# Kernel tuning notes

Hardware: AMD Instinct MI355X
Metric: run time of the kernel (lower is better)

## Reference

```python
import jax, jax.numpy as jnp
import numpy as np

D_IN = 3072      # == d_out (code reshapes x directly into heads)
D_OUT = 3072
N_HEADS = 16
HEAD_DIM = D_OUT // N_HEADS          # 192
D_C = D_OUT // 3                     # 1024, compressed latent dim
LN_EPS = 1e-5


def setup_inputs() -> dict:
    key = jax.random.key(0)
    ks = jax.random.split(key, 8)
    s = 0.02
    return {
        "x": jax.random.normal(ks[0], (2, 2048, D_IN), dtype=jnp.float32),
        "W_query": jax.random.normal(ks[1], (D_OUT, D_IN), dtype=jnp.float32) * s,
        "W_kv": jax.random.normal(ks[2], (D_C, D_IN), dtype=jnp.float32) * s,
        "W_uk": jax.random.normal(ks[3], (D_OUT, D_C), dtype=jnp.float32) * s,
        "W_uv": jax.random.normal(ks[4], (D_OUT, D_C), dtype=jnp.float32) * s,
        "W_out": jax.random.normal(ks[5], (D_OUT, D_OUT), dtype=jnp.float32) * s,
        "b_out": jnp.zeros((D_OUT,), dtype=jnp.float32),
        "ln_g": jnp.ones((D_C,), dtype=jnp.float32),
        "ln_b": jnp.zeros((D_C,), dtype=jnp.float32),
    }


def reference(x, W_query, W_kv, W_uk, W_uv, W_out, b_out, ln_g, ln_b):
    B, T, D = x.shape
    past_length = 0  # prefill, kv_cache=None

    # absorbed K projection: (d_out, d_in) @ (d_out, d_c) -> (H, head_dim, d_c)
    absorbed_k = (W_query @ W_uk).reshape(N_HEADS, HEAD_DIM, D_C)

    # compressed latent c_kv = LayerNorm(x @ W_kv^T), shape (B, S, d_c)
    c = x @ W_kv.T
    mu = jnp.mean(c, axis=-1, keepdims=True)
    var = jnp.mean(jnp.square(c - mu), axis=-1, keepdims=True)
    c_kv = (c - mu) * jax.lax.rsqrt(var + LN_EPS) * ln_g + ln_b
    S = c_kv.shape[1]

    # values decompressed: (B, S, H, head_dim)
    v = (c_kv @ W_uv.T).reshape(B, S, N_HEADS, HEAD_DIM)

    # queries: raw x reshaped into heads (as in the original code)
    q = x.reshape(B, T, N_HEADS, HEAD_DIM)

    # scores in compressed space: q @ absorbed_k @ c_kv^T
    tmp = jnp.einsum("bthd,hdc->bhtc", q, absorbed_k)           # (B,H,T,d_c)
    scores = jnp.einsum("bhtc,bsc->bhts", tmp, c_kv)
    scores = scores / np.float32(np.sqrt(HEAD_DIM))

    # causal mask with past_length offset (tril diagonal=past_length)
    row = jnp.arange(T)[:, None]
    col = jnp.arange(S)[None, :]
    mask = col <= (row + past_length)                            # (T,S) bool
    scores = jnp.where(mask[None, None], scores, -jnp.inf)

    weights = jax.nn.softmax(scores, axis=-1)                    # (B,H,T,S)

    ctx = jnp.einsum("bhts,bshd->bthd", weights, v).reshape(B, T, D_OUT)
    out = ctx @ W_out.T + b_out
    return out, c_kv
```

## Files before the change

kernel.cpp:

```cpp
#include <hip/hip_runtime.h>
#include <hip/hip_bf16.h>
#include <math.h>

#define BB 2
#define TT 2048
#define DD 3072
#define NH 16
#define HD 192
#define DC 1024

typedef __attribute__((ext_vector_type(8))) short bh8;
typedef __attribute__((ext_vector_type(4))) float f32x4;
typedef unsigned int u32;

__device__ __forceinline__ short f2b(float f) {
  __hip_bfloat16 h = __float2bfloat16(f);
  return *reinterpret_cast<short*>(&h);
}

__device__ __forceinline__ void gload16(const void* g, void* lds) {
  __builtin_amdgcn_global_load_lds(
      (const __attribute__((address_space(1))) u32*)g,
      (__attribute__((address_space(3))) u32*)lds, 16, 0, 0);
}

__global__ __launch_bounds__(256) void cast_f2b_k(const float* __restrict__ in,
                                                  short* __restrict__ out) {
  size_t i = ((size_t)blockIdx.x * 256 + threadIdx.x) * 8;
  float4 v0 = *(const float4*)&in[i];
  float4 v1 = *(const float4*)&in[i + 4];
  bh8 o;
  o[0] = f2b(v0.x); o[1] = f2b(v0.y); o[2] = f2b(v0.z); o[3] = f2b(v0.w);
  o[4] = f2b(v1.x); o[5] = f2b(v1.y); o[6] = f2b(v1.z); o[7] = f2b(v1.w);
  *(bh8*)&out[i] = o;
}

__global__ __launch_bounds__(256) void sum_cast_k(const float* __restrict__ p0,
                                                  const float* __restrict__ p1,
                                                  short* __restrict__ out) {
  size_t i = ((size_t)blockIdx.x * 256 + threadIdx.x) * 8;
  float4 a0 = *(const float4*)&p0[i];
  float4 a1 = *(const float4*)&p0[i + 4];
  float4 b0 = *(const float4*)&p1[i];
  float4 b1 = *(const float4*)&p1[i + 4];
  bh8 o;
  o[0] = f2b(a0.x + b0.x); o[1] = f2b(a0.y + b0.y);
  o[2] = f2b(a0.z + b0.z); o[3] = f2b(a0.w + b0.w);
  o[4] = f2b(a1.x + b1.x); o[5] = f2b(a1.y + b1.y);
  o[6] = f2b(a1.z + b1.z); o[7] = f2b(a1.w + b1.w);
  *(bh8*)&out[i] = o;
}

__global__ __launch_bounds__(256) void castT_f2b_k(const float* __restrict__ in,
                                                   short* __restrict__ out,
                                                   int R, int C) {
  __shared__ float t[64][65];
  const int cx = blockIdx.x * 64, ry = blockIdx.y * 64;
  const int tid = threadIdx.x, lx = tid & 15, ly = tid >> 4;
#pragma unroll
  for (int i = 0; i < 4; ++i) {
    int r = ly + i * 16;
    float4 v = *(const float4*)&in[(size_t)(ry + r) * C + cx + lx * 4];
    t[r][lx * 4 + 0] = v.x; t[r][lx * 4 + 1] = v.y;
    t[r][lx * 4 + 2] = v.z; t[r][lx * 4 + 3] = v.w;
  }
  __syncthreads();
#pragma unroll
  for (int i = 0; i < 4; ++i) {
    int c = ly + i * 16;
    ushort4 v;
    v.x = (unsigned short)f2b(t[lx * 4 + 0][c]);
    v.y = (unsigned short)f2b(t[lx * 4 + 1][c]);
    v.z = (unsigned short)f2b(t[lx * 4 + 2][c]);
    v.w = (unsigned short)f2b(t[lx * 4 + 3][c]);
    *(ushort4*)&out[(size_t)(cx + c) * R + ry + lx * 4] = v;
  }
}

template <int OUTMODE, bool BIAS>
__global__ __launch_bounds__(256) void gemm_bf16(
    const short* __restrict__ A, const short* __restrict__ Bt,
    const float* __restrict__ bias, void* __restrict__ Cout,
    int M, int N, int Klen, int lda, int ldb, size_t zoff_bytes) {
  __shared__ short As[8192];
  __shared__ short Bs[8192];
  const int tid = threadIdx.x;
  const int w = tid >> 6, l = tid & 63, lm = l & 15, lg = l >> 4;
  const int wr = w >> 1, wc = w & 1;

  const int bz = blockIdx.z;
  A += (size_t)bz * Klen;
  Bt += (size_t)bz * Klen;
  Cout = (void*)((char*)Cout + (size_t)bz * zoff_bytes);

  const int nwg = gridDim.x * gridDim.y;
  const int flat = blockIdx.y * gridDim.x + blockIdx.x;
  const int wgid = (flat & 7) * (nwg >> 3) + (flat >> 3);
  const int m0 = (wgid / gridDim.x) * 128, n0 = (wgid % gridDim.x) * 128;

  f32x4 acc[4][4] = {};

  for (int k0 = 0; k0 < Klen; k0 += 64) {
    __syncthreads();
#pragma unroll
    for (int c = 0; c < 4; ++c) {
      int p = c * 256 + w * 64 + l;
      int row = p >> 3, kc = p & 7;
      int g = kc ^ (row & 7);
      gload16(&A[(size_t)(m0 + row) * lda + k0 + g * 8],
              &As[(c * 256 + w * 64) * 8]);
      gload16(&Bt[(size_t)(n0 + row) * ldb + k0 + g * 8],
              &Bs[(c * 256 + w * 64) * 8]);
    }
    __syncthreads();

#pragma unroll
    for (int kh = 0; kh < 2; ++kh) {
      bh8 a[4], b[4];
#pragma unroll
      for (int mi = 0; mi < 4; ++mi) {
        int r = wr * 64 + mi * 16 + lm;
        a[mi] = *(const bh8*)&As[r * 64 + (((kh * 4 + lg) ^ (r & 7)) << 3)];
      }
#pragma unroll
      for (int ni = 0; ni < 4; ++ni) {
        int r = wc * 64 + ni * 16 + lm;
        b[ni] = *(const bh8*)&Bs[r * 64 + (((kh * 4 + lg) ^ (r & 7)) << 3)];
      }
#pragma unroll
      for (int mi = 0; mi < 4; ++mi)
#pragma unroll
        for (int ni = 0; ni < 4; ++ni)
          acc[mi][ni] = __builtin_amdgcn_mfma_f32_16x16x32_bf16(
              a[mi], b[ni], acc[mi][ni], 0, 0, 0);
    }
  }

#pragma unroll
  for (int mi = 0; mi < 4; ++mi) {
#pragma unroll
    for (int ni = 0; ni < 4; ++ni) {
      int row = m0 + wr * 64 + mi * 16 + lg * 4;
      int col = n0 + wc * 64 + ni * 16 + lm;
      float bi = 0.f;
      if (BIAS) bi = bias[col];
      if (OUTMODE == 2) {
        int b = row >> 11, t = row & 2047;
        ushort4 o;
        o.x = (unsigned short)f2b(acc[mi][ni][0]);
        o.y = (unsigned short)f2b(acc[mi][ni][1]);
        o.z = (unsigned short)f2b(acc[mi][ni][2]);
        o.w = (unsigned short)f2b(acc[mi][ni][3]);
        *(ushort4*)&((short*)Cout)[((size_t)(b * DD + col)) * TT + t] = o;
      } else {
#pragma unroll
        for (int r = 0; r < 4; ++r) {
          float v = acc[mi][ni][r] + bi;
          if (OUTMODE == 1)
            ((short*)Cout)[(size_t)(row + r) * N + col] = f2b(v);
          else
            ((float*)Cout)[(size_t)(row + r) * N + col] = v;
        }
      }
    }
  }
}

__global__ __launch_bounds__(256) void ln_k(const float* __restrict__ cp0,
                                            const float* __restrict__ cp1,
                                            const float* __restrict__ g,
                                            const float* __restrict__ bta,
                                            float* __restrict__ o32,
                                            short* __restrict__ o16) {
  const int row = blockIdx.x;
  const int tid = threadIdx.x;
  __shared__ float red1[4];
  __shared__ float red2[4];

  float4 va = *(const float4*)&cp0[(size_t)row * DC + tid * 4];
  float4 vb = *(const float4*)&cp1[(size_t)row * DC + tid * 4];
  float4 v;
  v.x = va.x + vb.x; v.y = va.y + vb.y; v.z = va.z + vb.z; v.w = va.w + vb.w;
  float s = v.x + v.y + v.z + v.w;
#pragma unroll
  for (int mk = 32; mk; mk >>= 1) s += __shfl_xor(s, mk, 64);
  if ((tid & 63) == 0) red1[tid >> 6] = s;
  __syncthreads();
  float mu = (red1[0] + red1[1] + red1[2] + red1[3]) * (1.f / DC);

  float dx = v.x - mu, dy = v.y - mu, dz = v.z - mu, dw = v.w - mu;
  float s2 = dx * dx + dy * dy + dz * dz + dw * dw;
#pragma unroll
  for (int mk = 32; mk; mk >>= 1) s2 += __shfl_xor(s2, mk, 64);
  if ((tid & 63) == 0) red2[tid >> 6] = s2;
  __syncthreads();
  float var = (red2[0] + red2[1] + red2[2] + red2[3]) * (1.f / DC);
  float rs = rsqrtf(var + 1e-5f);

  float4 gg = *(const float4*)&g[tid * 4];
  float4 bb = *(const float4*)&bta[tid * 4];
  float4 o;
  o.x = dx * rs * gg.x + bb.x;
  o.y = dy * rs * gg.y + bb.y;
  o.z = dz * rs * gg.z + bb.z;
  o.w = dw * rs * gg.w + bb.w;
  *(float4*)&o32[(size_t)row * DC + tid * 4] = o;
  ushort4 ob;
  ob.x = (unsigned short)f2b(o.x); ob.y = (unsigned short)f2b(o.y);
  ob.z = (unsigned short)f2b(o.z); ob.w = (unsigned short)f2b(o.w);
  *(ushort4*)&o16[(size_t)row * DC + tid * 4] = ob;
}

__global__ __launch_bounds__(256) void attn_mfma(
    const short* __restrict__ xb, const short* __restrict__ kf,
    const short* __restrict__ vT, short* __restrict__ ctx) {
  __shared__ short Ks[64 * 192];
  __shared__ short Vs[192 * 64];
  __shared__ short Ps[4][16 * 64];

  const int idx = blockIdx.x;
  const int qt = 31 - (idx >> 5);
  const int bh = idx & 31;
  const int h = bh & 15, b = bh >> 4;
  const int tid = threadIdx.x, w = tid >> 6, l = tid & 63;
  const int lm = l & 15, lg = l >> 4;
  const int qw0 = qt * 64 + w * 16;
  const float QS = 0.07216878364870323f;

  bh8 qf[6];
  {
    const short* qrow = &xb[(size_t)(b * TT + qw0 + lm) * DD + h * HD];
#pragma unroll
    for (int kq = 0; kq < 6; ++kq)
      qf[kq] = *(const bh8*)&qrow[kq * 32 + lg * 8];
  }

  f32x4 o[12] = {};
  float mrun[4], lrun[4];
#pragma unroll
  for (int r = 0; r < 4; ++r) { mrun[r] = -INFINITY; lrun[r] = 0.f; }

  for (int st = 0; st <= qt; ++st) {
    const int s0 = st * 64;
    __syncthreads();
#pragma unroll
    for (int c = 0; c < 6; ++c) {
      int p = c * 256 + w * 64 + l;
      {
        int krow = p / 24, kc = p - krow * 24;
        int g = kc ^ (krow & 7);
        gload16(&kf[(size_t)(b * TT + s0 + krow) * DD + h * HD + g * 8],
                &Ks[(c * 256 + w * 64) * 8]);
      }
      {
        int vrow = p >> 3, vc = p & 7;
        int gv = vc ^ (vrow & 7);
        gload16(&vT[(size_t)((b * NH + h) * HD + vrow) * TT + s0 + gv * 8],
                &Vs[(c * 256 + w * 64) * 8]);
      }
    }
    __syncthreads();

    f32x4 s[4] = {};
    __builtin_amdgcn_s_setprio(1);
#pragma unroll
    for (int nf = 0; nf < 4; ++nf) {
      const int krow = nf * 16 + lm;
      const short* kr = &Ks[krow * 192];
#pragma unroll
      for (int kq = 0; kq < 6; ++kq) {
        bh8 kb = *(const bh8*)&kr[(((kq * 4 + lg) ^ (krow & 7)) << 3)];
        s[nf] = __builtin_amdgcn_mfma_f32_16x16x32_bf16(qf[kq], kb, s[nf],
                                                        0, 0, 0);
      }
    }
    __builtin_amdgcn_s_setprio(0);

    float pv[4][4];
#pragma unroll
    for (int nf = 0; nf < 4; ++nf)
#pragma unroll
      for (int r = 0; r < 4; ++r) pv[nf][r] = s[nf][r] * QS;
    if (st == qt) {
#pragma unroll
      for (int nf = 0; nf < 4; ++nf)
#pragma unroll
        for (int r = 0; r < 4; ++r)
          if (nf * 16 + lm > w * 16 + lg * 4 + r) pv[nf][r] = -INFINITY;
    }
#pragma unroll
    for (int r = 0; r < 4; ++r) {
      float mt = fmaxf(fmaxf(pv[0][r], pv[1][r]), fmaxf(pv[2][r], pv[3][r]));
#pragma unroll
      for (int mk = 1; mk < 16; mk <<= 1) mt = fmaxf(mt, __shfl_xor(mt, mk));
      float mnew = fmaxf(mrun[r], mt);
      float corr = __expf(mrun[r] - mnew);
      mrun[r] = mnew;
      float ls = 0.f;
#pragma unroll
      for (int nf = 0; nf < 4; ++nf) {
        float p = __expf(pv[nf][r] - mnew);
        pv[nf][r] = p;
        ls += p;
      }
#pragma unroll
      for (int mk = 1; mk < 16; mk <<= 1) ls += __shfl_xor(ls, mk);
      lrun[r] = lrun[r] * corr + ls;
#pragma unroll
      for (int nf = 0; nf < 12; ++nf) o[nf][r] *= corr;
    }
#pragma unroll
    for (int nf = 0; nf < 4; ++nf)
#pragma unroll
      for (int r = 0; r < 4; ++r) {
        int prow = lg * 4 + r;
        int col = nf * 16 + lm;
        int sc = (((col >> 3) ^ (prow & 7)) << 3) + (col & 7);
        Ps[w][prow * 64 + sc] = f2b(pv[nf][r]);
      }

    bh8 pa0, pa1;
    {
      int prow = lm;
      pa0 = *(const bh8*)&Ps[w][prow * 64 + ((lg ^ (prow & 7)) << 3)];
      pa1 = *(const bh8*)&Ps[w][prow * 64 + (((4 + lg) ^ (prow & 7)) << 3)];
    }
    __builtin_amdgcn_s_setprio(1);
#pragma unroll
    for (int nf = 0; nf < 12; ++nf) {
      int drow = nf * 16 + lm;
      const short* vr = &Vs[drow * 64];
      bh8 vb0 = *(const bh8*)&vr[((lg ^ (drow & 7)) << 3)];
      bh8 vb1 = *(const bh8*)&vr[(((4 + lg) ^ (drow & 7)) << 3)];
      o[nf] = __builtin_amdgcn_mfma_f32_16x16x32_bf16(pa0, vb0, o[nf], 0, 0, 0);
      o[nf] = __builtin_amdgcn_mfma_f32_16x16x32_bf16(pa1, vb1, o[nf], 0, 0, 0);
    }
    __builtin_amdgcn_s_setprio(0);
  }

#pragma unroll
  for (int r = 0; r < 4; ++r) {
    float inv = 1.f / lrun[r];
    int row = qw0 + lg * 4 + r;
    short* cp = &ctx[(size_t)(b * TT + row) * DD + h * HD];
#pragma unroll
    for (int nf = 0; nf < 12; ++nf)
      cp[nf * 16 + lm] = f2b(o[nf][r] * inv);
  }
}

extern "C" void kernel_launch(void* const* d_in, const int* in_sizes, int n_in,
                              void* d_out, int out_size, void* d_ws,
                              size_t ws_size, hipStream_t stream) {
  const float* x    = (const float*)d_in[0];
  const float* Wq   = (const float*)d_in[1];
  const float* Wkv  = (const float*)d_in[2];
  const float* Wuk  = (const float*)d_in[3];
  const float* Wuv  = (const float*)d_in[4];
  const float* Wout = (const float*)d_in[5];
  const float* bout = (const float*)d_in[6];
  const float* lng  = (const float*)d_in[7];
  const float* lnb  = (const float*)d_in[8];

  float* out   = (float*)d_out;
  float* ckv32 = out + (size_t)BB * TT * DD;

  char* W = (char*)d_ws;
  short* xb     = (short*)(W);
  short* wbuf   = (short*)(W + 25165824);
  short* wukT   = (short*)(W + 44040192);
  short* wkvb   = (short*)(W + 50331648);
  short* wuvb   = (short*)(W + 56623104);
  short* akb    = (short*)(W + 62914560);
  float* cpre0  = (float*)(W + 69206016);
  short* ckvb   = (short*)(W + 85983232);
  short* kfullb = (short*)(W + 94371840);
  float* g1p0   = (float*)(W + 94371840);
  short* ctxb   = (short*)(W + 119537664);
  float* g1p1   = (float*)(W + 119537664);
  float* cpre1  = (float*)(W + 144703488);
  short* vTb    = (short*)(W + 144703488);
  const size_t G1_ZOFF = (size_t)(119537664 - 94371840);
  const size_t G2_ZOFF = (size_t)(144703488 - 69206016);

  cast_f2b_k<<<6144, 256, 0, stream>>>(x, xb);
  cast_f2b_k<<<4608, 256, 0, stream>>>(Wq, wbuf);
  cast_f2b_k<<<1536, 256, 0, stream>>>(Wkv, wkvb);
  cast_f2b_k<<<1536, 256, 0, stream>>>(Wuv, wuvb);
  castT_f2b_k<<<dim3(16, 48), 256, 0, stream>>>(Wuk, wukT, 3072, 1024);

  gemm_bf16<0, false><<<dim3(8, 24, 2), 256, 0, stream>>>(
      wbuf, wukT, nullptr, g1p0, 3072, 1024, 1536, 3072, 3072, G1_ZOFF);
  sum_cast_k<<<1536, 256, 0, stream>>>(g1p0, g1p1, akb);
  cast_f2b_k<<<4608, 256, 0, stream>>>(Wout, wbuf);
  gemm_bf16<0, false><<<dim3(8, 32, 2), 256, 0, stream>>>(
      xb, wkvb, nullptr, cpre0, 4096, 1024, 1536, 3072, 3072, G2_ZOFF);
  ln_k<<<4096, 256, 0, stream>>>(cpre0, cpre1, lng, lnb, ckv32, ckvb);
  gemm_bf16<1, false><<<dim3(24, 32), 256, 0, stream>>>(
      ckvb, akb, nullptr, kfullb, 4096, 3072, 1024, 1024, 1024, 0);
  gemm_bf16<2, false><<<dim3(24, 32), 256, 0, stream>>>(
      ckvb, wuvb, nullptr, vTb, 4096, 3072, 1024, 1024, 1024, 0);
  attn_mfma<<<1024, 256, 0, stream>>>(xb, kfullb, vTb, ctxb);
  gemm_bf16<0, true><<<dim3(24, 32), 256, 0, stream>>>(
      ctxb, wbuf, bout, out, 4096, 3072, 3072, 3072, 3072, 0);
}
```

Measured before the change: 399.8 us.

## Merge K/V decompression GEMMs and use exp2 with lazy softmax rescaling

The two separate GEMMs that expand the latent into K and V are replaced by one launch over a doubled N dimension. Tiles with n0 below 3072 write V transposed, and tiles above write K row-major. The attention kernel folds log2(e) into the score scale so it can use exp2f. It also skips the running-max correction and output rescale unless some lane's new max exceeds the old one by more than 8. The goal is to cut one launch and tail effect, and to remove most per-tile rescaling multiplies and exponentials. This relies on the akb weights sitting directly after wuvb in memory, and it trades some headroom in the fp32 accumulators for the skipped rescales.

```diff
diff --git a/kernel.cpp b/kernel.cpp
--- a/kernel.cpp
+++ b/kernel.cpp
@@ -81,6 +81,7 @@
 __global__ __launch_bounds__(256) void gemm_bf16(
     const short* __restrict__ A, const short* __restrict__ Bt,
     const float* __restrict__ bias, void* __restrict__ Cout,
+    void* __restrict__ Cout2,
     int M, int N, int Klen, int lda, int ldb, size_t zoff_bytes) {
   __shared__ short As[8192];
   __shared__ short Bs[8192];
@@ -144,14 +145,21 @@
       int col = n0 + wc * 64 + ni * 16 + lm;
       float bi = 0.f;
       if (BIAS) bi = bias[col];
-      if (OUTMODE == 2) {
-        int b = row >> 11, t = row & 2047;
-        ushort4 o;
-        o.x = (unsigned short)f2b(acc[mi][ni][0]);
-        o.y = (unsigned short)f2b(acc[mi][ni][1]);
-        o.z = (unsigned short)f2b(acc[mi][ni][2]);
-        o.w = (unsigned short)f2b(acc[mi][ni][3]);
-        *(ushort4*)&((short*)Cout)[((size_t)(b * DD + col)) * TT + t] = o;
+      if (OUTMODE == 3) {
+        if (n0 < 3072) {
+          int b = row >> 11, t = row & 2047;
+          ushort4 o4;
+          o4.x = (unsigned short)f2b(acc[mi][ni][0]);
+          o4.y = (unsigned short)f2b(acc[mi][ni][1]);
+          o4.z = (unsigned short)f2b(acc[mi][ni][2]);
+          o4.w = (unsigned short)f2b(acc[mi][ni][3]);
+          *(ushort4*)&((short*)Cout2)[((size_t)(b * DD + col)) * TT + t] = o4;
+        } else {
+#pragma unroll
+          for (int r = 0; r < 4; ++r)
+            ((short*)Cout)[(size_t)(row + r) * DD + (col - 3072)] =
+                f2b(acc[mi][ni][r]);
+        }
       } else {
 #pragma unroll
         for (int r = 0; r < 4; ++r) {
@@ -225,7 +233,7 @@
   const int tid = threadIdx.x, w = tid >> 6, l = tid & 63;
   const int lm = l & 15, lg = l >> 4;
   const int qw0 = qt * 64 + w * 16;
-  const float QS = 0.07216878364870323f;
+  const float QS2 = 0.10411756672f;
 
   bh8 qf[6];
   {
@@ -280,7 +288,7 @@
 #pragma unroll
     for (int nf = 0; nf < 4; ++nf)
 #pragma unroll
-      for (int r = 0; r < 4; ++r) pv[nf][r] = s[nf][r] * QS;
+      for (int r = 0; r < 4; ++r) pv[nf][r] = s[nf][r] * QS2;
     if (st == qt) {
 #pragma unroll
       for (int nf = 0; nf < 4; ++nf)
@@ -293,21 +301,24 @@
       float mt = fmaxf(fmaxf(pv[0][r], pv[1][r]), fmaxf(pv[2][r], pv[3][r]));
 #pragma unroll
       for (int mk = 1; mk < 16; mk <<= 1) mt = fmaxf(mt, __shfl_xor(mt, mk));
-      float mnew = fmaxf(mrun[r], mt);
-      float corr = __expf(mrun[r] - mnew);
-      mrun[r] = mnew;
+      if (__any(mt > mrun[r] + 8.f)) {
+        float mnew = fmaxf(mrun[r], mt);
+        float corr = exp2f(mrun[r] - mnew);
+        mrun[r] = mnew;
+        lrun[r] *= corr;
+#pragma unroll
+        for (int nf = 0; nf < 12; ++nf) o[nf][r] *= corr;
+      }
       float ls = 0.f;
 #pragma unroll
       for (int nf = 0; nf < 4; ++nf) {
-        float p = __expf(pv[nf][r] - mnew);
+        float p = exp2f(pv[nf][r] - mrun[r]);
         pv[nf][r] = p;
         ls += p;
       }
 #pragma unroll
       for (int mk = 1; mk < 16; mk <<= 1) ls += __shfl_xor(ls, mk);
-      lrun[r] = lrun[r] * corr + ls;
-#pragma unroll
-      for (int nf = 0; nf < 12; ++nf) o[nf][r] *= corr;
+      lrun[r] += ls;
     }
 #pragma unroll
     for (int nf = 0; nf < 4; ++nf)
@@ -390,17 +401,17 @@
   castT_f2b_k<<<dim3(16, 48), 256, 0, stream>>>(Wuk, wukT, 3072, 1024);
 
   gemm_bf16<0, false><<<dim3(8, 24, 2), 256, 0, stream>>>(
-      wbuf, wukT, nullptr, g1p0, 3072, 1024, 1536, 3072, 3072, G1_ZOFF);
+      wbuf, wukT, nullptr, g1p0, nullptr, 3072, 1024, 1536, 3072, 3072,
+      G1_ZOFF);
   sum_cast_k<<<1536, 256, 0, stream>>>(g1p0, g1p1, akb);
   cast_f2b_k<<<4608, 256, 0, stream>>>(Wout, wbuf);
   gemm_bf16<0, false><<<dim3(8, 32, 2), 256, 0, stream>>>(
-      xb, wkvb, nullptr, cpre0, 4096, 1024, 1536, 3072, 3072, G2_ZOFF);
+      xb, wkvb, nullptr, cpre0, nullptr, 4096, 1024, 1536, 3072, 3072,
+      G2_ZOFF);
   ln_k<<<4096, 256, 0, stream>>>(cpre0, cpre1, lng, lnb, ckv32, ckvb);
-  gemm_bf16<1, false><<<dim3(24, 32), 256, 0, stream>>>(
-      ckvb, akb, nullptr, kfullb, 4096, 3072, 1024, 1024, 1024, 0);
-  gemm_bf16<2, false><<<dim3(24, 32), 256, 0, stream>>>(
-      ckvb, wuvb, nullptr, vTb, 4096, 3072, 1024, 1024, 1024, 0);
+  gemm_bf16<3, false><<<dim3(48, 32), 256, 0, stream>>>(
+      ckvb, wuvb, nullptr, kfullb, vTb, 4096, 6144, 1024, 1024, 1024, 0);
   attn_mfma<<<1024, 256, 0, stream>>>(xb, kfullb, vTb, ctxb);
   gemm_bf16<0, true><<<dim3(24, 32), 256, 0, stream>>>(
-      ctxb, wbuf, bout, out, 4096, 3072, 3072, 3072, 3072, 0);
-}
+      ctxb, wbuf, bout, out, nullptr, 4096, 3072, 3072, 3072, 3072, 0);
+}
```

Result: slower. 500.8 us (+25.3%).
